# Kernel tuning notes

Hardware: AMD Instinct MI355X
Metric: run time of the kernel (lower is better)

## Reference

```python
import jax, jax.numpy as jnp
import numpy as np

CUTOFF = 5.0
LOG2 = 0.6931471805599453

def ssp(x):
    # ShiftedSoftplus: softplus(x) - log(2)
    return jax.nn.softplus(x) - LOG2

def setup_inputs() -> dict:
    key = jax.random.key(0)
    ks = jax.random.split(key, 10)
    B, P, A, G, F, E = 2, 4096, 96, 1, 32, 20
    return {
        "scalar": jax.random.normal(ks[0], (B, A, G, F), jnp.float32),
        "scalar_reciever": jax.random.normal(ks[1], (B, P, G, F), jnp.float32),
        "expansion": jax.random.uniform(ks[2], (B, P, A, E), jnp.float32),
        "mask": jax.random.uniform(ks[3], (B, P, A, G), jnp.float32),
        "edge_distance": jax.random.uniform(ks[4], (B, P, A, 1), jnp.float32) * CUTOFF,
        "W1e": jax.random.normal(ks[5], (E, F), jnp.float32) * 0.1,
        "b1e": jnp.zeros((F,), jnp.float32),
        "W2e": jax.random.normal(ks[6], (F, F), jnp.float32) * 0.1,
        "b2e": jnp.zeros((F,), jnp.float32),
        "W1n": jax.random.normal(ks[7], (2 * F, F), jnp.float32) * 0.1,
        "b1n": jnp.zeros((F,), jnp.float32),
        "W2n": jax.random.normal(ks[8], (F, F), jnp.float32) * 0.1,
        "b2n": jnp.zeros((F,), jnp.float32),
    }

def reference(scalar, scalar_reciever, expansion, mask, edge_distance,
              W1e, b1e, W2e, b2e, W1n, b1n, W2n, b2n):
    F = scalar.shape[-1]
    # edge gate: 2-layer MLP on expansion, times soft cutoff  -> [B,P,A,F]
    gates = ssp(expansion @ W1e + b1e) @ W2e + b2e
    gates = gates * (1.0 - jax.nn.sigmoid(5.0 * (edge_distance - (CUTOFF - 1.5))))
    # pairwise node MLP: split first linear into source/target halves instead of
    # materializing the [B,P,A,G,2F] repeat+concat tensor (same math).
    Ws, Wt = W1n[:F], W1n[F:]
    src = jnp.einsum('bagf,fh->bagh', scalar, Ws)            # [B,A,G,H]
    tgt = jnp.einsum('bpgf,fh->bpgh', scalar_reciever, Wt)   # [B,P,G,H]
    h = src[:, None, :, :, :] + tgt[:, :, None, :, :] + b1n  # [B,P,A,G,H]
    nodes = ssp(h) @ W2n + b2n                               # [B,P,A,G,F]
    result = mask[..., None] * (gates[..., None, :] * nodes)
    return jnp.sum(result, axis=-3)                          # sum over atoms A -> [B,P,G,F]

if __name__ == "__main__":
    out = reference(**setup_inputs())
    print(out.shape)
```

## Files before the change

kernel.cpp:

```cpp
#include <hip/hip_runtime.h>

#define NB   2
#define NP   4096
#define NA   96
#define NF   32
#define NE   20
#define NBP  (NB*NP)

typedef __attribute__((ext_vector_type(8)))  short bf16x8;
typedef __attribute__((ext_vector_type(16))) float f32x16;

union Frag { bf16x8 v; int i[4]; };

__device__ __forceinline__ int cvtpk(float lo, float hi) {
  int r;
  asm("v_cvt_pk_bf16_f32 %0, %1, %2" : "=v"(r) : "v"(lo), "v"(hi));
  return r;
}
__device__ __forceinline__ float ssp_f(float x) {
  float t = __expf(-fabsf(x));
  return fmaxf(x, 0.0f) + __logf(1.0f + t) - 0.69314718056f;
}
__device__ __forceinline__ f32x16 mfma32(const Frag a, const Frag b, f32x16 c) {
  return __builtin_amdgcn_mfma_f32_32x32x16_bf16(a.v, b.v, c, 0, 0, 0);
}
__device__ __forceinline__ f32x16 ld_bias16(const float* base ) {
  const float4* p = reinterpret_cast<const float4*>(base);
  float4 q0 = p[0], q1 = p[2], q2 = p[4], q3 = p[6];
  f32x16 c;
  c[0]=q0.x;  c[1]=q0.y;  c[2]=q0.z;  c[3]=q0.w;
  c[4]=q1.x;  c[5]=q1.y;  c[6]=q1.z;  c[7]=q1.w;
  c[8]=q2.x;  c[9]=q2.y;  c[10]=q2.z; c[11]=q2.w;
  c[12]=q3.x; c[13]=q3.y; c[14]=q3.z; c[15]=q3.w;
  return c;
}

__global__ __launch_bounds__(256)
void prep_kernel(const float* __restrict__ scalar,
                 const float* __restrict__ sr,
                 const float* __restrict__ W1e,
                 const float* __restrict__ W2e,
                 const float* __restrict__ W2n,
                 const float* __restrict__ W1n,
                 const float* __restrict__ b1n,
                 float* __restrict__ tgt_out,
                 float* __restrict__ src_ws,
                 int4* __restrict__ ftab)
{
  const int blk = blockIdx.x;
  if (blk < 1048) {
    int i = blk * 256 + threadIdx.x;
    int f   = i & 31;
    int row = i >> 5;
    const float* x;
    const float* W;
    float acc;
    if (row < NBP) { x = sr + row * NF;             W = W1n + NF * NF; acc = 0.0f;   }
    else           { x = scalar + (row - NBP) * NF; W = W1n;           acc = b1n[f]; }
    float4 xv[8];
#pragma unroll
    for (int q = 0; q < 8; ++q) xv[q] = reinterpret_cast<const float4*>(x)[q];
#pragma unroll
    for (int q = 0; q < 8; ++q) {
      acc = fmaf(xv[q].x, W[(4 * q + 0) * NF + f], acc);
      acc = fmaf(xv[q].y, W[(4 * q + 1) * NF + f], acc);
      acc = fmaf(xv[q].z, W[(4 * q + 2) * NF + f], acc);
      acc = fmaf(xv[q].w, W[(4 * q + 3) * NF + f], acc);
    }
    if (row < NBP) tgt_out[i] = acc;
    else           src_ws[(row - NBP) * NF + f] = acc;
  } else {
    int e = (blk - 1048) * 256 + threadIdx.x;
    if (e < 384) {
      const int f  = e >> 6;
      const int l  = e & 63;
      const int c  = l & 31;
      const int hw = l >> 5;
      const float* W = (f < 2) ? W1e : ((f < 4) ? W2e : W2n);
      const int kbase = (f & 1) ? (16 + 8 * hw) : (8 * hw);
      int4 v;
      int* vi = reinterpret_cast<int*>(&v);
#pragma unroll
      for (int r = 0; r < 4; ++r) {
        int ka = kbase + 2 * r, kb = ka + 1;
        bool pa = (f == 1) && (ka >= NE);
        bool pb = (f == 1) && (kb >= NE);
        float lo = W[(pa ? 0 : ka) * NF + c]; lo = pa ? 0.0f : lo;
        float hi = W[(pb ? 0 : kb) * NF + c]; hi = pb ? 0.0f : hi;
        vi[r] = cvtpk(lo, hi);
      }
      ftab[e] = v;
    }
  }
}

__global__ __launch_bounds__(256, 4)
void fused_main(const float* __restrict__ expansion,
                const float* __restrict__ mask,
                const float* __restrict__ edge_dist,
                const float* __restrict__ b1e,
                const float* __restrict__ b2e,
                const float* __restrict__ b2n,
                const float* __restrict__ src_ws,
                const int4* __restrict__ ftab,
                float* __restrict__ out)
{
  const int tid  = threadIdx.x;
  const int wid  = tid >> 6;
  const int lane = tid & 63;
  const int col  = lane & 31;
  const int hw   = lane >> 5;

  __shared__ __align__(16) float smb[96];
  if (tid < 32) {
    smb[tid]      = b1e[tid];
    smb[32 + tid] = b2e[tid];
    smb[64 + tid] = b2n[tid];
  }
  __syncthreads();
  const float* biasA = smb      + 4 * hw;
  const float* biasB = smb + 32 + 4 * hw;
  const float* biasC = smb + 64 + 4 * hw;

  Frag a1s0, a1s1, a2s0, a2s1, a3s0, a3s1;
  {
    int4 w0 = ftab[0 * 64 + lane];
    int4 w1 = ftab[1 * 64 + lane];
    int4 w2 = ftab[2 * 64 + lane];
    int4 w3 = ftab[3 * 64 + lane];
    int4 w4 = ftab[4 * 64 + lane];
    int4 w5 = ftab[5 * 64 + lane];
    a1s0.i[0]=w0.x; a1s0.i[1]=w0.y; a1s0.i[2]=w0.z; a1s0.i[3]=w0.w;
    a1s1.i[0]=w1.x; a1s1.i[1]=w1.y; a1s1.i[2]=w1.z; a1s1.i[3]=w1.w;
    a2s0.i[0]=w2.x; a2s0.i[1]=w2.y; a2s0.i[2]=w2.z; a2s0.i[3]=w2.w;
    a2s1.i[0]=w3.x; a2s1.i[1]=w3.y; a2s1.i[2]=w3.z; a2s1.i[3]=w3.w;
    a3s0.i[0]=w4.x; a3s0.i[1]=w4.y; a3s0.i[2]=w4.z; a3s0.i[3]=w4.w;
    a3s1.i[0]=w5.x; a3s1.i[1]=w5.y; a3s1.i[2]=w5.z; a3s1.i[3]=w5.w;
  }

  const int bp = blockIdx.x * 4 + wid;
  const int b  = bp >> 12;

  const float* tg = out + bp * NF;
  float4 t0 = *reinterpret_cast<const float4*>(tg + 8 * hw);
  float4 t1 = *reinterpret_cast<const float4*>(tg + 8 * hw + 4);
  float4 t2 = *reinterpret_cast<const float4*>(tg + 16 + 8 * hw);
  float4 t3 = *reinterpret_cast<const float4*>(tg + 16 + 8 * hw + 4);

  const float* expb  = expansion + (size_t)bp * (NA * NE);
  const float* maskb = mask      + bp * NA;
  const float* distb = edge_dist + bp * NA;
  const float* srcb  = src_ws    + b * (NA * NF);

  float4 ef[3][3];
  float  mk[3], dd[3];
#pragma unroll
  for (int t = 0; t < 3; ++t) {
    const int a = t * 32 + col;
    const float* ea = expb + a * NE;
    ef[t][0] = *reinterpret_cast<const float4*>(ea + 8 * hw);
    ef[t][1] = *reinterpret_cast<const float4*>(ea + 8 * hw + 4);
    ef[t][2] = *reinterpret_cast<const float4*>(ea + 16);
    mk[t] = maskb[a];
    dd[t] = distb[a];
  }
  float em[3];
#pragma unroll
  for (int t = 0; t < 3; ++t) {
    const float z = __expf(5.0f * (dd[t] - 3.5f));
    em[t] = mk[t] * __builtin_amdgcn_rcpf(1.0f + z);
  }

  f32x16 acc;
#pragma unroll
  for (int r = 0; r < 16; ++r) acc[r] = 0.0f;

#pragma unroll
  for (int t = 0; t < 3; ++t) {
    const int a = t * 32 + col;

    Frag b1f0, b1f1;
    b1f0.i[0] = cvtpk(ef[t][0].x, ef[t][0].y);
    b1f0.i[1] = cvtpk(ef[t][0].z, ef[t][0].w);
    b1f0.i[2] = cvtpk(ef[t][1].x, ef[t][1].y);
    b1f0.i[3] = cvtpk(ef[t][1].z, ef[t][1].w);
    b1f1.i[0] = hw ? 0 : cvtpk(ef[t][2].x, ef[t][2].y);
    b1f1.i[1] = hw ? 0 : cvtpk(ef[t][2].z, ef[t][2].w);
    b1f1.i[2] = 0;
    b1f1.i[3] = 0;

    f32x16 d1 = ld_bias16(biasA);
    d1 = mfma32(a1s0, b1f0, d1);
    d1 = mfma32(a1s1, b1f1, d1);
#pragma unroll
    for (int r = 0; r < 16; ++r) d1[r] = ssp_f(d1[r]);

    int u0 = cvtpk(d1[0],  d1[1]);
    int u1 = cvtpk(d1[2],  d1[3]);
    int u2 = cvtpk(d1[4],  d1[5]);
    int u3 = cvtpk(d1[6],  d1[7]);
    int u4 = cvtpk(d1[8],  d1[9]);
    int u5 = cvtpk(d1[10], d1[11]);
    int u6 = cvtpk(d1[12], d1[13]);
    int u7 = cvtpk(d1[14], d1[15]);
    asm("v_permlane32_swap_b32 %0, %1" : "+v"(u0), "+v"(u2));
    asm("v_permlane32_swap_b32 %0, %1" : "+v"(u1), "+v"(u3));
    asm("v_permlane32_swap_b32 %0, %1" : "+v"(u4), "+v"(u6));
    asm("v_permlane32_swap_b32 %0, %1" : "+v"(u5), "+v"(u7));
    Frag b2f0, b2f1;
    b2f0.i[0] = u0; b2f0.i[1] = u1; b2f0.i[2] = u2; b2f0.i[3] = u3;
    b2f1.i[0] = u4; b2f1.i[1] = u5; b2f1.i[2] = u6; b2f1.i[3] = u7;

    f32x16 d2 = ld_bias16(biasB);
    d2 = mfma32(a2s0, b2f0, d2);
    d2 = mfma32(a2s1, b2f1, d2);

    const float* sa = srcb + a * NF;
    float4 s0 = *reinterpret_cast<const float4*>(sa + 8 * hw);
    float4 s1 = *reinterpret_cast<const float4*>(sa + 8 * hw + 4);
    float4 s2 = *reinterpret_cast<const float4*>(sa + 16 + 8 * hw);
    float4 s3 = *reinterpret_cast<const float4*>(sa + 16 + 8 * hw + 4);
    Frag b3f0, b3f1;
    b3f0.i[0] = cvtpk(ssp_f(s0.x + t0.x), ssp_f(s0.y + t0.y));
    b3f0.i[1] = cvtpk(ssp_f(s0.z + t0.z), ssp_f(s0.w + t0.w));
    b3f0.i[2] = cvtpk(ssp_f(s1.x + t1.x), ssp_f(s1.y + t1.y));
    b3f0.i[3] = cvtpk(ssp_f(s1.z + t1.z), ssp_f(s1.w + t1.w));
    b3f1.i[0] = cvtpk(ssp_f(s2.x + t2.x), ssp_f(s2.y + t2.y));
    b3f1.i[1] = cvtpk(ssp_f(s2.z + t2.z), ssp_f(s2.w + t2.w));
    b3f1.i[2] = cvtpk(ssp_f(s3.x + t3.x), ssp_f(s3.y + t3.y));
    b3f1.i[3] = cvtpk(ssp_f(s3.z + t3.z), ssp_f(s3.w + t3.w));

    f32x16 d3 = ld_bias16(biasC);
    d3 = mfma32(a3s0, b3f0, d3);
    d3 = mfma32(a3s1, b3f1, d3);

#pragma unroll
    for (int r = 0; r < 16; ++r) acc[r] = fmaf(em[t] * d2[r], d3[r], acc[r]);
  }

#pragma unroll
  for (int m = 1; m <= 16; m <<= 1) {
#pragma unroll
    for (int r = 0; r < 16; ++r) acc[r] += __shfl_xor(acc[r], m, 64);
  }

  if (col == 0) {
    float4* o = reinterpret_cast<float4*>(out + bp * NF);
#pragma unroll
    for (int q = 0; q < 4; ++q) {
      float4 v;
      v.x = acc[4 * q];     v.y = acc[4 * q + 1];
      v.z = acc[4 * q + 2]; v.w = acc[4 * q + 3];
      o[2 * q + hw] = v;
    }
  }
}

extern "C" void kernel_launch(void* const* d_in, const int* in_sizes, int n_in,
                              void* d_out, int out_size, void* d_ws, size_t ws_size,
                              hipStream_t stream) {
  const float* scalar    = (const float*)d_in[0];
  const float* sreciever = (const float*)d_in[1];
  const float* expansion = (const float*)d_in[2];
  const float* maskp     = (const float*)d_in[3];
  const float* edist     = (const float*)d_in[4];
  const float* W1e       = (const float*)d_in[5];
  const float* b1e       = (const float*)d_in[6];
  const float* W2e       = (const float*)d_in[7];
  const float* b2e       = (const float*)d_in[8];
  const float* W1n       = (const float*)d_in[9];
  const float* b1n       = (const float*)d_in[10];
  const float* W2n       = (const float*)d_in[11];
  const float* b2n       = (const float*)d_in[12];
  float* out    = (float*)d_out;
  float* src_ws = (float*)d_ws;
  int4*  ftab   = (int4*)((char*)d_ws + 192 * NF * 4);

  prep_kernel<<<1050, 256, 0, stream>>>(scalar, sreciever, W1e, W2e, W2n,
                                        W1n, b1n, out, src_ws, ftab);
  fused_main<<<NBP / 4, 256, 0, stream>>>(expansion, maskp, edist,
                                          b1e, b2e, b2n, src_ws, ftab, out);
}
```

Baseline: 158.6 us.

## Split each output row's atom loop across three waves with atomic accumulation

Each wave now handles one 32-atom tile of one (b,p) row instead of looping over all three tiles. The grid grows threefold, and partial results are combined with atomicAdd into an output zeroed by a memset. The target projection moves from the output buffer to a separate workspace so the output can be cleared first. This aims to raise parallelism and shorten per-wave serial latency, at the cost of triple weight-fragment loads, an extra memset launch, and 16 atomics per half-wave per row.

```diff
diff --git a/kernel.cpp b/kernel.cpp
--- a/kernel.cpp
+++ b/kernel.cpp
@@ -43,7 +43,7 @@
                  const float* __restrict__ W2n,
                  const float* __restrict__ W1n,
                  const float* __restrict__ b1n,
-                 float* __restrict__ tgt_out,
+                 float* __restrict__ tgt_ws,
                  float* __restrict__ src_ws,
                  int4* __restrict__ ftab)
 {
@@ -67,7 +67,7 @@
       acc = fmaf(xv[q].z, W[(4 * q + 2) * NF + f], acc);
       acc = fmaf(xv[q].w, W[(4 * q + 3) * NF + f], acc);
     }
-    if (row < NBP) tgt_out[i] = acc;
+    if (row < NBP) tgt_ws[i] = acc;
     else           src_ws[(row - NBP) * NF + f] = acc;
   } else {
     int e = (blk - 1048) * 256 + threadIdx.x;
@@ -95,15 +95,16 @@
 }
 
 __global__ __launch_bounds__(256, 4)
-void fused_main(const float* __restrict__ expansion,
-                const float* __restrict__ mask,
-                const float* __restrict__ edge_dist,
-                const float* __restrict__ b1e,
-                const float* __restrict__ b2e,
-                const float* __restrict__ b2n,
-                const float* __restrict__ src_ws,
-                const int4* __restrict__ ftab,
-                float* __restrict__ out)
+void fused_t(const float* __restrict__ expansion,
+             const float* __restrict__ mask,
+             const float* __restrict__ edge_dist,
+             const float* __restrict__ b1e,
+             const float* __restrict__ b2e,
+             const float* __restrict__ b2n,
+             const float* __restrict__ src_ws,
+             const float* __restrict__ tgt_ws,
+             const int4* __restrict__ ftab,
+             float* __restrict__ out)
 {
   const int tid  = threadIdx.x;
   const int wid  = tid >> 6;
@@ -118,141 +119,103 @@
     smb[64 + tid] = b2n[tid];
   }
   __syncthreads();
-  const float* biasA = smb      + 4 * hw;
-  const float* biasB = smb + 32 + 4 * hw;
-  const float* biasC = smb + 64 + 4 * hw;
-
-  Frag a1s0, a1s1, a2s0, a2s1, a3s0, a3s1;
-  {
-    int4 w0 = ftab[0 * 64 + lane];
-    int4 w1 = ftab[1 * 64 + lane];
-    int4 w2 = ftab[2 * 64 + lane];
-    int4 w3 = ftab[3 * 64 + lane];
-    int4 w4 = ftab[4 * 64 + lane];
-    int4 w5 = ftab[5 * 64 + lane];
-    a1s0.i[0]=w0.x; a1s0.i[1]=w0.y; a1s0.i[2]=w0.z; a1s0.i[3]=w0.w;
-    a1s1.i[0]=w1.x; a1s1.i[1]=w1.y; a1s1.i[2]=w1.z; a1s1.i[3]=w1.w;
-    a2s0.i[0]=w2.x; a2s0.i[1]=w2.y; a2s0.i[2]=w2.z; a2s0.i[3]=w2.w;
-    a2s1.i[0]=w3.x; a2s1.i[1]=w3.y; a2s1.i[2]=w3.z; a2s1.i[3]=w3.w;
-    a3s0.i[0]=w4.x; a3s0.i[1]=w4.y; a3s0.i[2]=w4.z; a3s0.i[3]=w4.w;
-    a3s1.i[0]=w5.x; a3s1.i[1]=w5.y; a3s1.i[2]=w5.z; a3s1.i[3]=w5.w;
-  }
-
-  const int bp = blockIdx.x * 4 + wid;
-  const int b  = bp >> 12;
-
-  const float* tg = out + bp * NF;
+
+  const unsigned w  = blockIdx.x * 4 + wid;
+  const unsigned bp = w / 3u;
+  const int      t  = (int)(w - 3u * bp);
+  const int      b  = (int)(bp >> 12);
+  const int      a  = t * 32 + col;
+
+  const float* ea = expansion + (size_t)bp * (NA * NE) + a * NE;
+  float4 e0 = *reinterpret_cast<const float4*>(ea + 8 * hw);
+  float4 e1 = *reinterpret_cast<const float4*>(ea + 8 * hw + 4);
+  float4 e2 = *reinterpret_cast<const float4*>(ea + 16);
+  Frag b1f0, b1f1;
+  b1f0.i[0] = cvtpk(e0.x, e0.y);
+  b1f0.i[1] = cvtpk(e0.z, e0.w);
+  b1f0.i[2] = cvtpk(e1.x, e1.y);
+  b1f0.i[3] = cvtpk(e1.z, e1.w);
+  b1f1.i[0] = hw ? 0 : cvtpk(e2.x, e2.y);
+  b1f1.i[1] = hw ? 0 : cvtpk(e2.z, e2.w);
+  b1f1.i[2] = 0;
+  b1f1.i[3] = 0;
+
+  Frag aw;
+  f32x16 d1 = ld_bias16(smb + 4 * hw);
+  { int4 q = ftab[0 * 64 + lane]; aw.i[0]=q.x; aw.i[1]=q.y; aw.i[2]=q.z; aw.i[3]=q.w; }
+  d1 = mfma32(aw, b1f0, d1);
+  { int4 q = ftab[1 * 64 + lane]; aw.i[0]=q.x; aw.i[1]=q.y; aw.i[2]=q.z; aw.i[3]=q.w; }
+  d1 = mfma32(aw, b1f1, d1);
+#pragma unroll
+  for (int r = 0; r < 16; ++r) d1[r] = ssp_f(d1[r]);
+
+  int u0 = cvtpk(d1[0],  d1[1]);
+  int u1 = cvtpk(d1[2],  d1[3]);
+  int u2 = cvtpk(d1[4],  d1[5]);
+  int u3 = cvtpk(d1[6],  d1[7]);
+  int u4 = cvtpk(d1[8],  d1[9]);
+  int u5 = cvtpk(d1[10], d1[11]);
+  int u6 = cvtpk(d1[12], d1[13]);
+  int u7 = cvtpk(d1[14], d1[15]);
+  asm("v_permlane32_swap_b32 %0, %1" : "+v"(u0), "+v"(u2));
+  asm("v_permlane32_swap_b32 %0, %1" : "+v"(u1), "+v"(u3));
+  asm("v_permlane32_swap_b32 %0, %1" : "+v"(u4), "+v"(u6));
+  asm("v_permlane32_swap_b32 %0, %1" : "+v"(u5), "+v"(u7));
+  Frag b2f0, b2f1;
+  b2f0.i[0] = u0; b2f0.i[1] = u1; b2f0.i[2] = u2; b2f0.i[3] = u3;
+  b2f1.i[0] = u4; b2f1.i[1] = u5; b2f1.i[2] = u6; b2f1.i[3] = u7;
+
+  f32x16 d2 = ld_bias16(smb + 32 + 4 * hw);
+  { int4 q = ftab[2 * 64 + lane]; aw.i[0]=q.x; aw.i[1]=q.y; aw.i[2]=q.z; aw.i[3]=q.w; }
+  d2 = mfma32(aw, b2f0, d2);
+  { int4 q = ftab[3 * 64 + lane]; aw.i[0]=q.x; aw.i[1]=q.y; aw.i[2]=q.z; aw.i[3]=q.w; }
+  d2 = mfma32(aw, b2f1, d2);
+
+  const float mk = mask[bp * NA + a];
+  const float dd = edge_dist[bp * NA + a];
+  const float z  = __expf(5.0f * (dd - 3.5f));
+  const float em = mk * __builtin_amdgcn_rcpf(1.0f + z);
+
+  const float* sa = src_ws + (b * NA + a) * NF;
+  const float* tg = tgt_ws + bp * NF;
+  float4 s0 = *reinterpret_cast<const float4*>(sa + 8 * hw);
+  float4 s1 = *reinterpret_cast<const float4*>(sa + 8 * hw + 4);
+  float4 s2 = *reinterpret_cast<const float4*>(sa + 16 + 8 * hw);
+  float4 s3 = *reinterpret_cast<const float4*>(sa + 16 + 8 * hw + 4);
   float4 t0 = *reinterpret_cast<const float4*>(tg + 8 * hw);
   float4 t1 = *reinterpret_cast<const float4*>(tg + 8 * hw + 4);
   float4 t2 = *reinterpret_cast<const float4*>(tg + 16 + 8 * hw);
   float4 t3 = *reinterpret_cast<const float4*>(tg + 16 + 8 * hw + 4);
-
-  const float* expb  = expansion + (size_t)bp * (NA * NE);
-  const float* maskb = mask      + bp * NA;
-  const float* distb = edge_dist + bp * NA;
-  const float* srcb  = src_ws    + b * (NA * NF);
-
-  float4 ef[3][3];
-  float  mk[3], dd[3];
-#pragma unroll
-  for (int t = 0; t < 3; ++t) {
-    const int a = t * 32 + col;
-    const float* ea = expb + a * NE;
-    ef[t][0] = *reinterpret_cast<const float4*>(ea + 8 * hw);
-    ef[t][1] = *reinterpret_cast<const float4*>(ea + 8 * hw + 4);
-    ef[t][2] = *reinterpret_cast<const float4*>(ea + 16);
-    mk[t] = maskb[a];
-    dd[t] = distb[a];
-  }
-  float em[3];
-#pragma unroll
-  for (int t = 0; t < 3; ++t) {
-    const float z = __expf(5.0f * (dd[t] - 3.5f));
-    em[t] = mk[t] * __builtin_amdgcn_rcpf(1.0f + z);
-  }
-
-  f32x16 acc;
-#pragma unroll
-  for (int r = 0; r < 16; ++r) acc[r] = 0.0f;
-
-#pragma unroll
-  for (int t = 0; t < 3; ++t) {
-    const int a = t * 32 + col;
-
-    Frag b1f0, b1f1;
-    b1f0.i[0] = cvtpk(ef[t][0].x, ef[t][0].y);
-    b1f0.i[1] = cvtpk(ef[t][0].z, ef[t][0].w);
-    b1f0.i[2] = cvtpk(ef[t][1].x, ef[t][1].y);
-    b1f0.i[3] = cvtpk(ef[t][1].z, ef[t][1].w);
-    b1f1.i[0] = hw ? 0 : cvtpk(ef[t][2].x, ef[t][2].y);
-    b1f1.i[1] = hw ? 0 : cvtpk(ef[t][2].z, ef[t][2].w);
-    b1f1.i[2] = 0;
-    b1f1.i[3] = 0;
-
-    f32x16 d1 = ld_bias16(biasA);
-    d1 = mfma32(a1s0, b1f0, d1);
-    d1 = mfma32(a1s1, b1f1, d1);
-#pragma unroll
-    for (int r = 0; r < 16; ++r) d1[r] = ssp_f(d1[r]);
-
-    int u0 = cvtpk(d1[0],  d1[1]);
-    int u1 = cvtpk(d1[2],  d1[3]);
-    int u2 = cvtpk(d1[4],  d1[5]);
-    int u3 = cvtpk(d1[6],  d1[7]);
-    int u4 = cvtpk(d1[8],  d1[9]);
-    int u5 = cvtpk(d1[10], d1[11]);
-    int u6 = cvtpk(d1[12], d1[13]);
-    int u7 = cvtpk(d1[14], d1[15]);
-    asm("v_permlane32_swap_b32 %0, %1" : "+v"(u0), "+v"(u2));
-    asm("v_permlane32_swap_b32 %0, %1" : "+v"(u1), "+v"(u3));
-    asm("v_permlane32_swap_b32 %0, %1" : "+v"(u4), "+v"(u6));
-    asm("v_permlane32_swap_b32 %0, %1" : "+v"(u5), "+v"(u7));
-    Frag b2f0, b2f1;
-    b2f0.i[0] = u0; b2f0.i[1] = u1; b2f0.i[2] = u2; b2f0.i[3] = u3;
-    b2f1.i[0] = u4; b2f1.i[1] = u5; b2f1.i[2] = u6; b2f1.i[3] = u7;
-
-    f32x16 d2 = ld_bias16(biasB);
-    d2 = mfma32(a2s0, b2f0, d2);
-    d2 = mfma32(a2s1, b2f1, d2);
-
-    const float* sa = srcb + a * NF;
-    float4 s0 = *reinterpret_cast<const float4*>(sa + 8 * hw);
-    float4 s1 = *reinterpret_cast<const float4*>(sa + 8 * hw + 4);
-    float4 s2 = *reinterpret_cast<const float4*>(sa + 16 + 8 * hw);
-    float4 s3 = *reinterpret_cast<const float4*>(sa + 16 + 8 * hw + 4);
-    Frag b3f0, b3f1;
-    b3f0.i[0] = cvtpk(ssp_f(s0.x + t0.x), ssp_f(s0.y + t0.y));
-    b3f0.i[1] = cvtpk(ssp_f(s0.z + t0.z), ssp_f(s0.w + t0.w));
-    b3f0.i[2] = cvtpk(ssp_f(s1.x + t1.x), ssp_f(s1.y + t1.y));
-    b3f0.i[3] = cvtpk(ssp_f(s1.z + t1.z), ssp_f(s1.w + t1.w));
-    b3f1.i[0] = cvtpk(ssp_f(s2.x + t2.x), ssp_f(s2.y + t2.y));
-    b3f1.i[1] = cvtpk(ssp_f(s2.z + t2.z), ssp_f(s2.w + t2.w));
-    b3f1.i[2] = cvtpk(ssp_f(s3.x + t3.x), ssp_f(s3.y + t3.y));
-    b3f1.i[3] = cvtpk(ssp_f(s3.z + t3.z), ssp_f(s3.w + t3.w));
-
-    f32x16 d3 = ld_bias16(biasC);
-    d3 = mfma32(a3s0, b3f0, d3);
-    d3 = mfma32(a3s1, b3f1, d3);
-
-#pragma unroll
-    for (int r = 0; r < 16; ++r) acc[r] = fmaf(em[t] * d2[r], d3[r], acc[r]);
-  }
+  Frag b3f0, b3f1;
+  b3f0.i[0] = cvtpk(ssp_f(s0.x + t0.x), ssp_f(s0.y + t0.y));
+  b3f0.i[1] = cvtpk(ssp_f(s0.z + t0.z), ssp_f(s0.w + t0.w));
+  b3f0.i[2] = cvtpk(ssp_f(s1.x + t1.x), ssp_f(s1.y + t1.y));
+  b3f0.i[3] = cvtpk(ssp_f(s1.z + t1.z), ssp_f(s1.w + t1.w));
+  b3f1.i[0] = cvtpk(ssp_f(s2.x + t2.x), ssp_f(s2.y + t2.y));
+  b3f1.i[1] = cvtpk(ssp_f(s2.z + t2.z), ssp_f(s2.w + t2.w));
+  b3f1.i[2] = cvtpk(ssp_f(s3.x + t3.x), ssp_f(s3.y + t3.y));
+  b3f1.i[3] = cvtpk(ssp_f(s3.z + t3.z), ssp_f(s3.w + t3.w));
+
+  f32x16 d3 = ld_bias16(smb + 64 + 4 * hw);
+  { int4 q = ftab[4 * 64 + lane]; aw.i[0]=q.x; aw.i[1]=q.y; aw.i[2]=q.z; aw.i[3]=q.w; }
+  d3 = mfma32(aw, b3f0, d3);
+  { int4 q = ftab[5 * 64 + lane]; aw.i[0]=q.x; aw.i[1]=q.y; aw.i[2]=q.z; aw.i[3]=q.w; }
+  d3 = mfma32(aw, b3f1, d3);
+
+#pragma unroll
+  for (int r = 0; r < 16; ++r) d3[r] = em * d2[r] * d3[r];
 
 #pragma unroll
   for (int m = 1; m <= 16; m <<= 1) {
 #pragma unroll
-    for (int r = 0; r < 16; ++r) acc[r] += __shfl_xor(acc[r], m, 64);
+    for (int r = 0; r < 16; ++r) d3[r] += __shfl_xor(d3[r], m, 64);
   }
 
   if (col == 0) {
-    float4* o = reinterpret_cast<float4*>(out + bp * NF);
-#pragma unroll
-    for (int q = 0; q < 4; ++q) {
-      float4 v;
-      v.x = acc[4 * q];     v.y = acc[4 * q + 1];
-      v.z = acc[4 * q + 2]; v.w = acc[4 * q + 3];
-      o[2 * q + hw] = v;
-    }
+    float* o = out + bp * NF + 4 * hw;
+#pragma unroll
+    for (int r = 0; r < 16; ++r)
+      atomicAdd(o + ((r & 3) + 8 * (r >> 2)), d3[r]);
   }
 }
 
@@ -274,10 +237,12 @@
   const float* b2n       = (const float*)d_in[12];
   float* out    = (float*)d_out;
   float* src_ws = (float*)d_ws;
-  int4*  ftab   = (int4*)((char*)d_ws + 192 * NF * 4);
-
+  int4*  ftab   = (int4*)((char*)d_ws + 24576);
+  float* tgt_ws = (float*)((char*)d_ws + 24576 + 6144);
+
+  hipMemsetAsync(out, 0, (size_t)out_size * sizeof(float), stream);
   prep_kernel<<<1050, 256, 0, stream>>>(scalar, sreciever, W1e, W2e, W2n,
-                                        W1n, b1n, out, src_ws, ftab);
-  fused_main<<<NBP / 4, 256, 0, stream>>>(expansion, maskp, edist,
-                                          b1e, b2e, b2n, src_ws, ftab, out);
-}
+                                        W1n, b1n, tgt_ws, src_ws, ftab);
+  fused_t<<<6144, 256, 0, stream>>>(expansion, maskp, edist,
+                                    b1e, b2e, b2n, src_ws, tgt_ws, ftab, out);
+}
```

After: 153.2 us. -3.4%, faster.
